# Kernel optimization log

Hardware: AMD Instinct MI355X
Metric: run time of the kernel (lower is better)

Reference implementation:

```python
import jax, jax.numpy as jnp
import numpy as np

# Module hyperparameters (init_kwargs)
D = 2          # input_dim
OUT = 3        # output_dim
T = 14         # log2 hash table size
L = 16         # number of levels
F = 2          # features per level
N_MIN, N_MAX = 16, 512
B = 1048576    # batch of query points
HIDDEN = 64

_b = np.exp((np.log(N_MAX) - np.log(N_MIN)) / (L - 1))
RES = jnp.asarray(np.floor(N_MIN * _b ** np.arange(L)).astype(np.float32))  # [L]

# voxel corner offsets [D, 2^D] (same construction as torch module)
_border = np.empty((D, 2 ** D), dtype=np.int32)
for _i in range(D):
    _border[_i, :] = np.array(([0] * 2 ** _i + [1] * 2 ** _i) * 2 ** (D - _i - 1), dtype=np.int32)
BORDER = jnp.asarray(_border)

# NVIDIA tiny-cuda-nn primes; uint32 arithmetic is exact for the low T bits
# (low 14 bits of a product/xor only depend on low 32 bits), matching torch's
# int64 multiply-xor followed by mod 2^T.
PRIMES = jnp.array([1, 2654435761, 805459861, 3674653429, 2097192037, 1434869437, 2165219737][:D], dtype=jnp.uint32)


def setup_inputs() -> dict:
    key = jax.random.key(0)
    ks = jax.random.split(key, 8)
    x = jax.random.uniform(ks[0], (B, D), jnp.float32)  # coords in [0,1)
    tables = jax.random.uniform(ks[1], (L, 2 ** T, F), jnp.float32, -1e-4, 1e-4)
    W1 = jax.random.normal(ks[2], (HIDDEN, L * F), jnp.float32) * 0.05
    b1 = jnp.zeros((HIDDEN,), jnp.float32)
    W2 = jax.random.normal(ks[3], (HIDDEN, HIDDEN), jnp.float32) * 0.05
    b2 = jnp.zeros((HIDDEN,), jnp.float32)
    W3 = jax.random.normal(ks[4], (OUT, HIDDEN), jnp.float32) * 0.05
    b3 = jnp.zeros((OUT,), jnp.float32)
    return {"x": x, "tables": tables, "W1": W1, "b1": b1, "W2": W2, "b2": b2, "W3": W3, "b3": b3}


def reference(x, tables, W1, b1, W2, b2, W3, b3):
    n = x.shape[0]
    # scale coords by each level resolution: [B, D, L]
    scaled = x[:, :, None] * RES[None, None, :]
    grid = jnp.floor(scaled).astype(jnp.int32)                     # [B, D, L]
    corners = grid[..., None] + BORDER[None, :, None, :]           # [B, D, L, 2^D]
    # spatial hash: xor of coord * prime per dimension, mod 2^T
    h = jnp.zeros((n, L, 2 ** D), jnp.uint32)
    for i in range(D):
        h = h ^ (corners[:, i].astype(jnp.uint32) * PRIMES[i])
    idx = (h & jnp.uint32(2 ** T - 1)).astype(jnp.int32)           # [B, L, 2^D]
    # per-level embedding gather: [B, L, 2^D, F]
    looked = tables[jnp.arange(L)[None, :, None], idx]
    # (bi/tri)linear interpolation weights: prod over dims -> [B, L, 2^D]
    w = jnp.prod(1.0 - jnp.abs(scaled[..., None] - corners.astype(x.dtype)), axis=1)
    feat = jnp.einsum('blc,blcf->blf', w, looked).reshape(n, L * F)  # [B, L*F]
    # small MLP head
    h1 = jax.nn.relu(feat @ W1.T + b1)
    h2 = jax.nn.relu(h1 @ W2.T + b2)
    return h2 @ W3.T + b3
```

## Files before the change

### kernel.cpp

```cpp
#include <hip/hip_runtime.h>
#include <hip/hip_bf16.h>
#include <math.h>


#define TBL_MASK 16383u
#define PRIME1   2654435761u

typedef __attribute__((ext_vector_type(8))) short short8;
typedef __attribute__((ext_vector_type(4))) float f32x4;
typedef __attribute__((ext_vector_type(4))) unsigned int uint4v;

struct ResArr { float r[16]; };

__device__ __forceinline__ unsigned short bf16rn(float f) {
    __hip_bfloat16 h = __float2bfloat16(f);
    return __builtin_bit_cast(unsigned short, h);
}
__device__ __forceinline__ float bf16tof(unsigned short u) {
    unsigned int xx = ((unsigned int)u) << 16;
    return __builtin_bit_cast(float, xx);
}
__device__ __forceinline__ short8 ld8(const unsigned short* p) {
    return __builtin_bit_cast(short8, *(const uint4v*)p);
}

#define MFMA(a, b, c) __builtin_amdgcn_mfma_f32_16x16x32_bf16((a), (b), (c), 0, 0, 0)

#define W1H_OFF 0
#define W1L_OFF 2048
#define W2H_OFF 4096
#define W2L_OFF 8192
#define W3H_OFF 12288
#define W3L_OFF 13312
#define WS_USHORTS 14336

__global__ __launch_bounds__(256) void split_weights(
    const float* __restrict__ W1, const float* __restrict__ W2,
    const float* __restrict__ W3, unsigned short* __restrict__ ws)
{
    const int t = blockIdx.x * blockDim.x + threadIdx.x;
    const int stride = gridDim.x * blockDim.x;
    for (int i = t; i < 2048; i += stride) {
        const float v = W1[i];
        const unsigned short hb = bf16rn(v);
        ws[W1H_OFF + i] = hb;
        ws[W1L_OFF + i] = bf16rn(v - bf16tof(hb));
    }
    for (int i = t; i < 4096; i += stride) {
        const float v = W2[i];
        const unsigned short hb = bf16rn(v);
        ws[W2H_OFF + i] = hb;
        ws[W2L_OFF + i] = bf16rn(v - bf16tof(hb));
    }
    for (int i = t; i < 1024; i += stride) {
        const float v = (i < 192) ? W3[i] : 0.0f;
        const unsigned short hb = bf16rn(v);
        ws[W3H_OFF + i] = hb;
        ws[W3L_OFF + i] = bf16rn(v - bf16tof(hb));
    }
}

__global__ __launch_bounds__(64, 3) void mh_mfma(
    const float* __restrict__ x,
    const float* __restrict__ tables,
    const unsigned short* __restrict__ wsw,
    const float* __restrict__ b1,
    const float* __restrict__ b2,
    const float* __restrict__ b3,
    float* __restrict__ out,
    ResArr res, int n)
{
    __shared__ __align__(16) unsigned short smem[5120];
    unsigned short* const sFH = smem;
    unsigned short* const sFL = smem + 2560;
    unsigned short* const sAH = smem;
    unsigned short* const sAL = smem + 2304;

    const int L  = threadIdx.x;
    const int ln = L & 15;
    const int q  = L >> 4;
    const long base = (long)blockIdx.x * 64;
    long s = base + L;
    if (s >= (long)n) s = (long)n - 1;

    const float2 xv = reinterpret_cast<const float2*>(x)[s];
    const float2* __restrict__ tbl2 = reinterpret_cast<const float2*>(tables);

    #pragma unroll 4
    for (int l = 0; l < 16; ++l) {
        const float r  = res.r[l];
        const float sx = xv.x * r;
        const float sy = xv.y * r;
        const float gx = floorf(sx);
        const float gy = floorf(sy);
        const unsigned ux = (unsigned)(int)gx;
        const unsigned uy = (unsigned)(int)gy;
        const unsigned hy0 = uy * PRIME1;
        const unsigned hy1 = hy0 + PRIME1;
        const unsigned i00 = ( ux       ^ hy0) & TBL_MASK;
        const unsigned i10 = ((ux + 1u) ^ hy0) & TBL_MASK;
        const unsigned i01 = ( ux       ^ hy1) & TBL_MASK;
        const unsigned i11 = ((ux + 1u) ^ hy1) & TBL_MASK;
        const float2* tl = tbl2 + (l << 14);
        const float2 t00 = tl[i00];
        const float2 t10 = tl[i10];
        const float2 t01 = tl[i01];
        const float2 t11 = tl[i11];
        const float wx0 = 1.0f - fabsf(sx - gx);
        const float wx1 = 1.0f - fabsf(sx - (gx + 1.0f));
        const float wy0 = 1.0f - fabsf(sy - gy);
        const float wy1 = 1.0f - fabsf(sy - (gy + 1.0f));
        const float w00 = wx0 * wy0;
        const float w10 = wx1 * wy0;
        const float w01 = wx0 * wy1;
        const float w11 = wx1 * wy1;
        const float f0 = fmaf(w00, t00.x, fmaf(w10, t10.x, fmaf(w01, t01.x, w11 * t11.x)));
        const float f1 = fmaf(w00, t00.y, fmaf(w10, t10.y, fmaf(w01, t01.y, w11 * t11.y)));
        const unsigned short h0 = bf16rn(f0);
        const unsigned short h1e = bf16rn(f1);
        const unsigned short l0 = bf16rn(f0 - bf16tof(h0));
        const unsigned short l1 = bf16rn(f1 - bf16tof(h1e));
        *(unsigned int*)&sFH[L * 40 + 2 * l] = (unsigned)h0 | ((unsigned)h1e << 16);
        *(unsigned int*)&sFL[L * 40 + 2 * l] = (unsigned)l0 | ((unsigned)l1 << 16);
    }

    short8 a1h[2][2], a1l[2][2];
    #pragma unroll
    for (int mh = 0; mh < 2; ++mh)
        #pragma unroll
        for (int mt = 0; mt < 2; ++mt) {
            const int row = mh * 32 + mt * 16 + ln;
            a1h[mh][mt] = ld8(&sFH[row * 40 + q * 8]);
            a1l[mh][mt] = ld8(&sFL[row * 40 + q * 8]);
        }

    float b1v[4], b2v[4];
    #pragma unroll
    for (int nt = 0; nt < 4; ++nt) { b1v[nt] = b1[nt * 16 + ln]; b2v[nt] = b2[nt * 16 + ln]; }
    const float b3v = (ln < 3) ? b3[ln] : 0.0f;

    const f32x4 zero4 = {0.0f, 0.0f, 0.0f, 0.0f};

    for (int mh = 0; mh < 2; ++mh) {
        f32x4 acc1[2][4];
        #pragma unroll
        for (int mt = 0; mt < 2; ++mt)
            #pragma unroll
            for (int nt = 0; nt < 4; ++nt) acc1[mt][nt] = zero4;

        #pragma unroll
        for (int nt = 0; nt < 4; ++nt) {
            const short8 bh = ld8(&wsw[W1H_OFF + (nt * 16 + ln) * 32 + q * 8]);
            const short8 bl = ld8(&wsw[W1L_OFF + (nt * 16 + ln) * 32 + q * 8]);
            #pragma unroll
            for (int mt = 0; mt < 2; ++mt) {
                f32x4 a = acc1[mt][nt];
                a = MFMA(a1l[mh][mt], bh, a);
                a = MFMA(a1h[mh][mt], bl, a);
                a = MFMA(a1h[mh][mt], bh, a);
                acc1[mt][nt] = a;
            }
        }
        #pragma unroll
        for (int mt = 0; mt < 2; ++mt)
            #pragma unroll
            for (int nt = 0; nt < 4; ++nt) {
                const int col = nt * 16 + ln;
                #pragma unroll
                for (int r = 0; r < 4; ++r) {
                    float v = fmaxf(acc1[mt][nt][r] + b1v[nt], 0.0f);
                    const unsigned short hb = bf16rn(v);
                    const unsigned short lb = bf16rn(v - bf16tof(hb));
                    const int rl = mt * 16 + q * 4 + r;
                    sAH[rl * 72 + col] = hb;
                    sAL[rl * 72 + col] = lb;
                }
            }

        short8 a2h[2][2], a2l[2][2];
        #pragma unroll
        for (int mt = 0; mt < 2; ++mt)
            #pragma unroll
            for (int ks = 0; ks < 2; ++ks) {
                const int row = mt * 16 + ln;
                a2h[mt][ks] = ld8(&sAH[row * 72 + ks * 32 + q * 8]);
                a2l[mt][ks] = ld8(&sAL[row * 72 + ks * 32 + q * 8]);
            }
        f32x4 acc2[2][4];
        #pragma unroll
        for (int mt = 0; mt < 2; ++mt)
            #pragma unroll
            for (int nt = 0; nt < 4; ++nt) acc2[mt][nt] = zero4;

        #pragma unroll
        for (int nt = 0; nt < 4; ++nt)
            #pragma unroll
            for (int ks = 0; ks < 2; ++ks) {
                const short8 bh = ld8(&wsw[W2H_OFF + (nt * 16 + ln) * 64 + ks * 32 + q * 8]);
                const short8 bl = ld8(&wsw[W2L_OFF + (nt * 16 + ln) * 64 + ks * 32 + q * 8]);
                #pragma unroll
                for (int mt = 0; mt < 2; ++mt) {
                    f32x4 a = acc2[mt][nt];
                    a = MFMA(a2l[mt][ks], bh, a);
                    a = MFMA(a2h[mt][ks], bl, a);
                    a = MFMA(a2h[mt][ks], bh, a);
                    acc2[mt][nt] = a;
                }
            }
        #pragma unroll
        for (int mt = 0; mt < 2; ++mt)
            #pragma unroll
            for (int nt = 0; nt < 4; ++nt) {
                const int col = nt * 16 + ln;
                #pragma unroll
                for (int r = 0; r < 4; ++r) {
                    float v = fmaxf(acc2[mt][nt][r] + b2v[nt], 0.0f);
                    const unsigned short hb = bf16rn(v);
                    const unsigned short lb = bf16rn(v - bf16tof(hb));
                    const int rl = mt * 16 + q * 4 + r;
                    sAH[rl * 72 + col] = hb;
                    sAL[rl * 72 + col] = lb;
                }
            }

        short8 a3h[2][2], a3l[2][2];
        #pragma unroll
        for (int mt = 0; mt < 2; ++mt)
            #pragma unroll
            for (int ks = 0; ks < 2; ++ks) {
                const int row = mt * 16 + ln;
                a3h[mt][ks] = ld8(&sAH[row * 72 + ks * 32 + q * 8]);
                a3l[mt][ks] = ld8(&sAL[row * 72 + ks * 32 + q * 8]);
            }
        f32x4 acc3[2] = {zero4, zero4};
        #pragma unroll
        for (int ks = 0; ks < 2; ++ks) {
            const short8 bh = ld8(&wsw[W3H_OFF + ln * 64 + ks * 32 + q * 8]);
            const short8 bl = ld8(&wsw[W3L_OFF + ln * 64 + ks * 32 + q * 8]);
            #pragma unroll
            for (int mt = 0; mt < 2; ++mt) {
                f32x4 a = acc3[mt];
                a = MFMA(a3l[mt][ks], bh, a);
                a = MFMA(a3h[mt][ks], bl, a);
                a = MFMA(a3h[mt][ks], bh, a);
                acc3[mt] = a;
            }
        }
        if (ln < 3) {
            #pragma unroll
            for (int mt = 0; mt < 2; ++mt)
                #pragma unroll
                for (int r = 0; r < 4; ++r) {
                    const long sg = base + mh * 32 + mt * 16 + q * 4 + r;
                    if (sg < (long)n) out[sg * 3 + ln] = acc3[mt][r] + b3v;
                }
        }
    }
}

extern "C" void kernel_launch(void* const* d_in, const int* in_sizes, int n_in,
                              void* d_out, int out_size, void* d_ws, size_t ws_size,
                              hipStream_t stream) {
    const float* x      = (const float*)d_in[0];
    const float* tables = (const float*)d_in[1];
    const float* W1     = (const float*)d_in[2];
    const float* b1v    = (const float*)d_in[3];
    const float* W2     = (const float*)d_in[4];
    const float* b2v    = (const float*)d_in[5];
    const float* W3     = (const float*)d_in[6];
    const float* b3v    = (const float*)d_in[7];
    float* out = (float*)d_out;
    unsigned short* wsu = (unsigned short*)d_ws;

    const int n = in_sizes[0] / 2;

    ResArr ra;
    const double bb = exp((log(512.0) - log(16.0)) / 15.0);
    for (int k = 0; k < 16; ++k) ra.r[k] = (float)floor(16.0 * pow(bb, (double)k));

    hipLaunchKernelGGL(split_weights, dim3(8), dim3(256), 0, stream, W1, W2, W3, wsu);

    dim3 grid((n + 63) / 64), block(64);
    hipLaunchKernelGGL(mh_mfma, grid, block, 0, stream,
                       x, tables, wsu, b1v, b2v, b3v, out, ra, n);
}
```

Before: 277.5 us.

## Split fused hash-encode+MLP kernel into separate encode and MLP kernels

Replaces the single fused kernel with two kernels when workspace is large enough. An encode kernel (256 threads per block) computes the hash-grid features and writes them as split hi/lo bf16 rows to global workspace. A second MFMA kernel then runs the three-layer MLP from that buffer. The aim is to give the gather-heavy encode and the MFMA-heavy MLP separate occupancy and launch shapes, at the cost of a 128-byte-per-point round trip through global memory (about 128 MB written and read).

```diff
diff --git a/kernel.cpp b/kernel.cpp
--- a/kernel.cpp
+++ b/kernel.cpp
@@ -57,6 +57,220 @@
         const unsigned short hb = bf16rn(v);
         ws[W3H_OFF + i] = hb;
         ws[W3L_OFF + i] = bf16rn(v - bf16tof(hb));
+    }
+}
+
+__global__ __launch_bounds__(256, 4) void mh_encode(
+    const float* __restrict__ x,
+    const float* __restrict__ tables,
+    unsigned short* __restrict__ feat,
+    ResArr res, int n)
+{
+    long s = (long)blockIdx.x * 256 + threadIdx.x;
+    if (s >= (long)n) s = (long)n - 1;
+
+    const float2 xv = reinterpret_cast<const float2*>(x)[s];
+    const float2* __restrict__ tbl2 = reinterpret_cast<const float2*>(tables);
+
+    unsigned int hiu[16], lou[16];
+
+    #pragma unroll
+    for (int l = 0; l < 16; ++l) {
+        const float r  = res.r[l];
+        const float sx = xv.x * r;
+        const float sy = xv.y * r;
+        const float gx = floorf(sx);
+        const float gy = floorf(sy);
+        const unsigned ux = (unsigned)(int)gx;
+        const unsigned uy = (unsigned)(int)gy;
+        const unsigned hy0 = uy * PRIME1;
+        const unsigned hy1 = hy0 + PRIME1;
+        const unsigned i00 = ( ux       ^ hy0) & TBL_MASK;
+        const unsigned i10 = ((ux + 1u) ^ hy0) & TBL_MASK;
+        const unsigned i01 = ( ux       ^ hy1) & TBL_MASK;
+        const unsigned i11 = ((ux + 1u) ^ hy1) & TBL_MASK;
+        const float2* tl = tbl2 + (l << 14);
+        const float2 t00 = tl[i00];
+        const float2 t10 = tl[i10];
+        const float2 t01 = tl[i01];
+        const float2 t11 = tl[i11];
+        const float wx0 = 1.0f - fabsf(sx - gx);
+        const float wx1 = 1.0f - fabsf(sx - (gx + 1.0f));
+        const float wy0 = 1.0f - fabsf(sy - gy);
+        const float wy1 = 1.0f - fabsf(sy - (gy + 1.0f));
+        const float w00 = wx0 * wy0;
+        const float w10 = wx1 * wy0;
+        const float w01 = wx0 * wy1;
+        const float w11 = wx1 * wy1;
+        const float f0 = fmaf(w00, t00.x, fmaf(w10, t10.x, fmaf(w01, t01.x, w11 * t11.x)));
+        const float f1 = fmaf(w00, t00.y, fmaf(w10, t10.y, fmaf(w01, t01.y, w11 * t11.y)));
+        const unsigned short h0 = bf16rn(f0);
+        const unsigned short h1e = bf16rn(f1);
+        const unsigned short l0 = bf16rn(f0 - bf16tof(h0));
+        const unsigned short l1 = bf16rn(f1 - bf16tof(h1e));
+        hiu[l] = (unsigned)h0 | ((unsigned)h1e << 16);
+        lou[l] = (unsigned)l0 | ((unsigned)l1 << 16);
+    }
+
+    uint4v* row = (uint4v*)(feat + (size_t)s * 64);
+    #pragma unroll
+    for (int c = 0; c < 4; ++c) {
+        uint4v vh = { hiu[c*4+0], hiu[c*4+1], hiu[c*4+2], hiu[c*4+3] };
+        row[c] = vh;
+    }
+    #pragma unroll
+    for (int c = 0; c < 4; ++c) {
+        uint4v vl = { lou[c*4+0], lou[c*4+1], lou[c*4+2], lou[c*4+3] };
+        row[4 + c] = vl;
+    }
+}
+
+__global__ __launch_bounds__(64, 4) void mh_mlp(
+    const unsigned short* __restrict__ feat,
+    const unsigned short* __restrict__ wsw,
+    const float* __restrict__ b1,
+    const float* __restrict__ b2,
+    const float* __restrict__ b3,
+    float* __restrict__ out, int n)
+{
+    __shared__ __align__(16) unsigned short sAH[32 * 72];
+    __shared__ __align__(16) unsigned short sAL[32 * 72];
+
+    const int L  = threadIdx.x;
+    const int ln = L & 15;
+    const int q  = L >> 4;
+    const long base = (long)blockIdx.x * 64;
+
+    float b1v[4], b2v[4];
+    #pragma unroll
+    for (int nt = 0; nt < 4; ++nt) { b1v[nt] = b1[nt * 16 + ln]; b2v[nt] = b2[nt * 16 + ln]; }
+    const float b3v = (ln < 3) ? b3[ln] : 0.0f;
+
+    const f32x4 zero4 = {0.0f, 0.0f, 0.0f, 0.0f};
+
+    for (int mh = 0; mh < 2; ++mh) {
+        short8 a1h[2], a1l[2];
+        #pragma unroll
+        for (int mt = 0; mt < 2; ++mt) {
+            long row = base + mh * 32 + mt * 16 + ln;
+            if (row >= (long)n) row = (long)n - 1;
+            const unsigned short* rp = feat + (size_t)row * 64;
+            a1h[mt] = ld8(rp + q * 8);
+            a1l[mt] = ld8(rp + 32 + q * 8);
+        }
+        f32x4 acc1[2][4];
+        #pragma unroll
+        for (int mt = 0; mt < 2; ++mt)
+            #pragma unroll
+            for (int nt = 0; nt < 4; ++nt) acc1[mt][nt] = zero4;
+
+        #pragma unroll
+        for (int nt = 0; nt < 4; ++nt) {
+            const short8 bh = ld8(&wsw[W1H_OFF + (nt * 16 + ln) * 32 + q * 8]);
+            const short8 bl = ld8(&wsw[W1L_OFF + (nt * 16 + ln) * 32 + q * 8]);
+            #pragma unroll
+            for (int mt = 0; mt < 2; ++mt) {
+                f32x4 a = acc1[mt][nt];
+                a = MFMA(a1l[mt], bh, a);
+                a = MFMA(a1h[mt], bl, a);
+                a = MFMA(a1h[mt], bh, a);
+                acc1[mt][nt] = a;
+            }
+        }
+        #pragma unroll
+        for (int mt = 0; mt < 2; ++mt)
+            #pragma unroll
+            for (int nt = 0; nt < 4; ++nt) {
+                const int col = nt * 16 + ln;
+                #pragma unroll
+                for (int r = 0; r < 4; ++r) {
+                    float v = fmaxf(acc1[mt][nt][r] + b1v[nt], 0.0f);
+                    const unsigned short hb = bf16rn(v);
+                    const unsigned short lb = bf16rn(v - bf16tof(hb));
+                    const int rl = mt * 16 + q * 4 + r;
+                    sAH[rl * 72 + col] = hb;
+                    sAL[rl * 72 + col] = lb;
+                }
+            }
+
+        short8 a2h[2][2], a2l[2][2];
+        #pragma unroll
+        for (int mt = 0; mt < 2; ++mt)
+            #pragma unroll
+            for (int ks = 0; ks < 2; ++ks) {
+                const int row = mt * 16 + ln;
+                a2h[mt][ks] = ld8(&sAH[row * 72 + ks * 32 + q * 8]);
+                a2l[mt][ks] = ld8(&sAL[row * 72 + ks * 32 + q * 8]);
+            }
+        f32x4 acc2[2][4];
+        #pragma unroll
+        for (int mt = 0; mt < 2; ++mt)
+            #pragma unroll
+            for (int nt = 0; nt < 4; ++nt) acc2[mt][nt] = zero4;
+
+        #pragma unroll
+        for (int nt = 0; nt < 4; ++nt)
+            #pragma unroll
+            for (int ks = 0; ks < 2; ++ks) {
+                const short8 bh = ld8(&wsw[W2H_OFF + (nt * 16 + ln) * 64 + ks * 32 + q * 8]);
+                const short8 bl = ld8(&wsw[W2L_OFF + (nt * 16 + ln) * 64 + ks * 32 + q * 8]);
+                #pragma unroll
+                for (int mt = 0; mt < 2; ++mt) {
+                    f32x4 a = acc2[mt][nt];
+                    a = MFMA(a2l[mt][ks], bh, a);
+                    a = MFMA(a2h[mt][ks], bl, a);
+                    a = MFMA(a2h[mt][ks], bh, a);
+                    acc2[mt][nt] = a;
+                }
+            }
+        #pragma unroll
+        for (int mt = 0; mt < 2; ++mt)
+            #pragma unroll
+            for (int nt = 0; nt < 4; ++nt) {
+                const int col = nt * 16 + ln;
+                #pragma unroll
+                for (int r = 0; r < 4; ++r) {
+                    float v = fmaxf(acc2[mt][nt][r] + b2v[nt], 0.0f);
+                    const unsigned short hb = bf16rn(v);
+                    const unsigned short lb = bf16rn(v - bf16tof(hb));
+                    const int rl = mt * 16 + q * 4 + r;
+                    sAH[rl * 72 + col] = hb;
+                    sAL[rl * 72 + col] = lb;
+                }
+            }
+
+        short8 a3h[2][2], a3l[2][2];
+        #pragma unroll
+        for (int mt = 0; mt < 2; ++mt)
+            #pragma unroll
+            for (int ks = 0; ks < 2; ++ks) {
+                const int row = mt * 16 + ln;
+                a3h[mt][ks] = ld8(&sAH[row * 72 + ks * 32 + q * 8]);
+                a3l[mt][ks] = ld8(&sAL[row * 72 + ks * 32 + q * 8]);
+            }
+        f32x4 acc3[2] = {zero4, zero4};
+        #pragma unroll
+        for (int ks = 0; ks < 2; ++ks) {
+            const short8 bh = ld8(&wsw[W3H_OFF + ln * 64 + ks * 32 + q * 8]);
+            const short8 bl = ld8(&wsw[W3L_OFF + ln * 64 + ks * 32 + q * 8]);
+            #pragma unroll
+            for (int mt = 0; mt < 2; ++mt) {
+                f32x4 a = acc3[mt];
+                a = MFMA(a3l[mt][ks], bh, a);
+                a = MFMA(a3h[mt][ks], bl, a);
+                a = MFMA(a3h[mt][ks], bh, a);
+                acc3[mt] = a;
+            }
+        }
+        if (ln < 3) {
+            #pragma unroll
+            for (int mt = 0; mt < 2; ++mt)
+                #pragma unroll
+                for (int r = 0; r < 4; ++r) {
+                    const long sg = base + mh * 32 + mt * 16 + q * 4 + r;
+                    if (sg < (long)n) out[sg * 3 + ln] = acc3[mt][r] + b3v;
+                }
+        }
     }
 }
 
@@ -280,7 +494,16 @@
 
     hipLaunchKernelGGL(split_weights, dim3(8), dim3(256), 0, stream, W1, W2, W3, wsu);
 
-    dim3 grid((n + 63) / 64), block(64);
-    hipLaunchKernelGGL(mh_mfma, grid, block, 0, stream,
-                       x, tables, wsu, b1v, b2v, b3v, out, ra, n);
-}
+    const size_t need = (size_t)WS_USHORTS * 2 + (size_t)n * 128;
+    if (ws_size >= need) {
+        unsigned short* featp = wsu + WS_USHORTS;
+        dim3 gE((n + 255) / 256), bE(256);
+        hipLaunchKernelGGL(mh_encode, gE, bE, 0, stream, x, tables, featp, ra, n);
+        dim3 gM((n + 63) / 64), bM(64);
+        hipLaunchKernelGGL(mh_mlp, gM, bM, 0, stream, featp, wsu, b1v, b2v, b3v, out, n);
+    } else {
+        dim3 grid((n + 63) / 64), block(64);
+        hipLaunchKernelGGL(mh_mfma, grid, block, 0, stream,
+                           x, tables, wsu, b1v, b2v, b3v, out, ra, n);
+    }
+}
```

Result: slower. 395.8 us (+42.6%).
